# Kernel tuning notes

Hardware: AMD Instinct MI355X
Metric: run time of the kernel (lower is better)

## Reference

```python
import jax, jax.numpy as jnp
import numpy as np

N = 50000      # nodes
E = 250000     # edges
D = 256        # in_channels
MSG = 256      # msg_dim
TD = 64        # time encoder out_channels
ED = MSG + TD  # edge_dim = 320
H = 4          # heads
C = 64         # out_channels // heads


def setup_inputs() -> dict:
    key = jax.random.key(0)
    ks = jax.random.split(key, 16)
    s_d = 1.0 / np.sqrt(D)
    s_e = 1.0 / np.sqrt(ED)
    return {
        "x": jax.random.normal(ks[0], (N, D), jnp.float32),
        "last_update": jax.random.uniform(ks[1], (N,), jnp.float32) * 1000.0,
        "t": jax.random.uniform(ks[2], (E,), jnp.float32) * 1000.0,
        "msg": jax.random.normal(ks[3], (E, MSG), jnp.float32),
        "edge_index": jax.random.randint(ks[4], (2, E), 0, N, jnp.int32),
        # TimeEncoder: Linear(1, TD) followed by cos
        "time_w": jax.random.normal(ks[5], (TD,), jnp.float32),
        "time_b": jax.random.normal(ks[6], (TD,), jnp.float32) * 0.1,
        # TransformerConv linears (weights stored [out, in] like torch)
        "Wq": jax.random.normal(ks[7], (H * C, D), jnp.float32) * s_d,
        "bq": jnp.zeros((H * C,), jnp.float32),
        "Wk": jax.random.normal(ks[8], (H * C, D), jnp.float32) * s_d,
        "bk": jnp.zeros((H * C,), jnp.float32),
        "Wv": jax.random.normal(ks[9], (H * C, D), jnp.float32) * s_d,
        "bv": jnp.zeros((H * C,), jnp.float32),
        "We": jax.random.normal(ks[10], (H * C, ED), jnp.float32) * s_e,  # lin_edge, no bias
        "Wskip": jax.random.normal(ks[11], (H * C, D), jnp.float32) * s_d,
        "bskip": jnp.zeros((H * C,), jnp.float32),
    }


def reference(x, last_update, t, msg, edge_index, time_w, time_b,
              Wq, bq, Wk, bk, Wv, bv, We, Wskip, bskip):
    src = edge_index[0]  # j: message source
    dst = edge_index[1]  # i: message target

    # time encoding: cos(Linear(1, TD)(rel_t))
    rel_t = last_update[src] - t                              # [E]
    rel_t_enc = jnp.cos(rel_t[:, None] * time_w[None, :] + time_b)  # [E, TD]
    edge_attr = jnp.concatenate([rel_t_enc, msg], axis=-1)    # [E, ED]

    # TransformerConv (heads=4, concat=True, root_weight=True, beta=False, eval mode)
    q = (x @ Wq.T + bq).reshape(N, H, C)
    k = (x @ Wk.T + bk).reshape(N, H, C)
    v = (x @ Wv.T + bv).reshape(N, H, C)
    e = (edge_attr @ We.T).reshape(E, H, C)

    k_j = k[src] + e                                           # [E, H, C]
    alpha = jnp.einsum('ehc,ehc->eh', q[dst], k_j) / np.sqrt(C)  # [E, H]

    # segment softmax over incoming edges of each target node
    m = jax.ops.segment_max(alpha, dst, num_segments=N)        # [N, H]
    m = jnp.where(jnp.isfinite(m), m, 0.0)
    ex = jnp.exp(alpha - m[dst])                               # [E, H]
    denom = jax.ops.segment_sum(ex, dst, num_segments=N)       # [N, H]
    alpha = ex / (denom[dst] + 1e-16)                          # [E, H]

    out_e = (v[src] + e) * alpha[:, :, None]                   # [E, H, C]
    out = jax.ops.segment_sum(out_e, dst, num_segments=N)      # [N, H, C]
    out = out.reshape(N, H * C) + (x @ Wskip.T + bskip)        # skip connection
    return out
```

## Files before the change

### kernel.cpp

```cpp
#include <hip/hip_runtime.h>
#include <math.h>

#define NN 50000
#define EE 250000
#define NPAD 50048

typedef float f32x4 __attribute__((ext_vector_type(4)));
typedef __bf16 bf16x8 __attribute__((ext_vector_type(8)));

static __device__ __forceinline__ ushort f2b(float f) {
    unsigned u = __float_as_uint(f);
    unsigned r = (u + 0x7FFFu + ((u >> 16) & 1u)) >> 16;
    return (ushort)r;
}
static __device__ __forceinline__ float b2f(ushort u) {
    return __uint_as_float(((unsigned)u) << 16);
}

__global__ void k_prep_w(const float* __restrict__ Wq, const float* __restrict__ bq,
                         const float* __restrict__ Wk, const float* __restrict__ bk,
                         const float* __restrict__ Wv, const float* __restrict__ bv,
                         const float* __restrict__ Wskip, const float* __restrict__ bskip,
                         const float* __restrict__ We,
                         ushort* __restrict__ Wnb, ushort* __restrict__ Web,
                         float* __restrict__ bcat) {
    int i = blockIdx.x * 256 + threadIdx.x;
    int st = gridDim.x * 256;
    for (int idx = i; idx < 1024 * 256; idx += st) {
        int n = idx >> 8, kk = idx & 255;
        int sel = n >> 8, o = n & 255;
        const float* W = (sel == 0) ? Wq : (sel == 1) ? Wk : (sel == 2) ? Wv : Wskip;
        Wnb[idx] = f2b(W[o * 256 + kk]);
    }
    for (int idx = i; idx < 256 * 320; idx += st) Web[idx] = f2b(We[idx]);
    for (int idx = i; idx < 1024; idx += st) {
        int sel = idx >> 8, o = idx & 255;
        const float* b = (sel == 0) ? bq : (sel == 1) ? bk : (sel == 2) ? bv : bskip;
        bcat[idx] = b[o];
    }
}

__global__ void k_zero(unsigned* __restrict__ deg) {
    int i = blockIdx.x * 256 + threadIdx.x;
    if (i < NN) deg[i] = 0u;
}

__global__ void k_hist(const int* __restrict__ ei, unsigned* __restrict__ deg) {
    int i = blockIdx.x * 256 + threadIdx.x;
    if (i < EE) atomicAdd(&deg[ei[EE + i]], 1u);
}

__global__ __launch_bounds__(1024) void k_scan(const unsigned* __restrict__ deg,
                                               unsigned* __restrict__ offs,
                                               unsigned* __restrict__ cursor) {
    __shared__ unsigned part[1024];
    int t = threadIdx.x;
    const int CH = (NN + 1023) / 1024;
    int b0 = t * CH;
    unsigned s = 0;
    for (int i = 0; i < CH; ++i) { int idx = b0 + i; if (idx < NN) s += deg[idx]; }
    part[t] = s;
    __syncthreads();
    for (int d = 1; d < 1024; d <<= 1) {
        unsigned v = (t >= d) ? part[t - d] : 0u;
        __syncthreads();
        part[t] += v;
        __syncthreads();
    }
    unsigned run = (t == 0) ? 0u : part[t - 1];
    for (int i = 0; i < CH; ++i) {
        int idx = b0 + i;
        if (idx < NN) { offs[idx] = run; cursor[idx] = run; run += deg[idx]; }
    }
    if (t == 1023) offs[NN] = EE;
}

__global__ void k_scatter(const int* __restrict__ ei, unsigned* __restrict__ cursor,
                          int* __restrict__ sorted_e) {
    int i = blockIdx.x * 256 + threadIdx.x;
    if (i < EE) {
        unsigned p = atomicAdd(&cursor[ei[EE + i]], 1u);
        sorted_e[p] = i;
    }
}

__global__ __launch_bounds__(256) void k_node_mfma(
        const float* __restrict__ x, const ushort* __restrict__ Wnb,
        const float* __restrict__ bcat,
        ushort* __restrict__ qb, ushort* __restrict__ kb, ushort* __restrict__ vb,
        float* __restrict__ out) {
    __shared__ ushort As[128 * 64];
    __shared__ ushort Bs[128 * 64];
    int tid = threadIdx.x;
    int lane = tid & 63, wid = tid >> 6;
    int wr = wid >> 1, wc = wid & 1;
    int li = lane & 15, g = lane >> 4;
    int bm = blockIdx.x, bn = blockIdx.y;
    f32x4 acc[4][4] = {};
    for (int k0 = 0; k0 < 256; k0 += 64) {
        __syncthreads();
        #pragma unroll
        for (int i = 0; i < 4; ++i) {
            int ch = tid + i * 256;
            int r = ch >> 3, c = ch & 7;
            int row = bm * 128 + r;
            union { ushort u[8]; uint4 v; } s;
            if (row < NN) {
                const float* xr = x + (size_t)row * 256 + k0 + c * 8;
                float4 a = *(const float4*)xr;
                float4 b = *(const float4*)(xr + 4);
                s.u[0] = f2b(a.x); s.u[1] = f2b(a.y); s.u[2] = f2b(a.z); s.u[3] = f2b(a.w);
                s.u[4] = f2b(b.x); s.u[5] = f2b(b.y); s.u[6] = f2b(b.z); s.u[7] = f2b(b.w);
            } else {
                s.v = make_uint4(0, 0, 0, 0);
            }
            *(uint4*)&As[r * 64 + ((c ^ (r & 7)) * 8)] = s.v;
            uint4 vb4 = *(const uint4*)(Wnb + (size_t)(bn * 128 + r) * 256 + k0 + c * 8);
            *(uint4*)&Bs[r * 64 + ((c ^ (r & 7)) * 8)] = vb4;
        }
        __syncthreads();
        #pragma unroll
        for (int kk = 0; kk < 2; ++kk) {
            bf16x8 a[4], b[4];
            #pragma unroll
            for (int m = 0; m < 4; ++m) {
                int r = wr * 64 + m * 16 + li;
                a[m] = *(const bf16x8*)&As[r * 64 + (((kk * 4 + g) ^ (r & 7)) * 8)];
            }
            #pragma unroll
            for (int n = 0; n < 4; ++n) {
                int r = wc * 64 + n * 16 + li;
                b[n] = *(const bf16x8*)&Bs[r * 64 + (((kk * 4 + g) ^ (r & 7)) * 8)];
            }
            #pragma unroll
            for (int m = 0; m < 4; ++m)
                #pragma unroll
                for (int n = 0; n < 4; ++n)
                    acc[m][n] = __builtin_amdgcn_mfma_f32_16x16x32_bf16(a[m], b[n], acc[m][n], 0, 0, 0);
        }
    }
    int sel = bn >> 1;
    int cbase = (bn & 1) * 128;
    ushort* dstb = (sel == 0) ? qb : (sel == 1) ? kb : vb;
    #pragma unroll
    for (int m = 0; m < 4; ++m) {
        #pragma unroll
        for (int r = 0; r < 4; ++r) {
            int row = bm * 128 + wr * 64 + m * 16 + g * 4 + r;
            if (row >= NN) continue;
            #pragma unroll
            for (int n = 0; n < 4; ++n) {
                int coll = wc * 64 + n * 16 + li;
                float val = acc[m][n][r] + bcat[bn * 128 + coll];
                int cin = cbase + coll;
                if (sel < 3) dstb[(size_t)row * 256 + cin] = f2b(val);
                else         out[(size_t)row * 256 + cin] = val;
            }
        }
    }
}

__global__ __launch_bounds__(256) void k_edge_mfma(
        const float* __restrict__ msg, const float* __restrict__ t_arr,
        const float* __restrict__ lu, const float* __restrict__ tw,
        const float* __restrict__ tb, const ushort* __restrict__ Web,
        const ushort* __restrict__ qb, const ushort* __restrict__ kb,
        const int* __restrict__ ei,
        ushort* __restrict__ ebuf, float* __restrict__ alpha) {
    __shared__ ushort SS[64 * 328];
    __shared__ int s_src[64], s_dst[64];
    __shared__ float s_relt[64];
    int tid = threadIdx.x;
    int lane = tid & 63, wid = tid >> 6;
    int wr = wid >> 1, wc = wid & 1;
    int li = lane & 15, g = lane >> 4;
    int e0 = blockIdx.x * 64;
    if (tid < 64) {
        int e = e0 + tid;
        if (e >= EE) e = EE - 1;
        int s = ei[e];
        s_src[tid] = s;
        s_dst[tid] = ei[EE + e];
        s_relt[tid] = lu[s] - t_arr[e];
    }
    f32x4 acc[2][8] = {};
    for (int k0 = 0; k0 < 320; k0 += 64) {
        __syncthreads();
        #pragma unroll
        for (int i = 0; i < 2; ++i) {
            int ch = tid + i * 256;
            int r = ch >> 3, c = ch & 7;
            union { ushort u[8]; uint4 v; } s;
            if (k0 == 0) {
                float rt = s_relt[r];
                #pragma unroll
                for (int j = 0; j < 8; ++j)
                    s.u[j] = f2b(cosf(rt * tw[c * 8 + j] + tb[c * 8 + j]));
            } else {
                int erow = e0 + r; if (erow >= EE) erow = EE - 1;
                const float* mrow = msg + (size_t)erow * 256 + (k0 - 64) + c * 8;
                float4 a = *(const float4*)mrow;
                float4 b = *(const float4*)(mrow + 4);
                s.u[0] = f2b(a.x); s.u[1] = f2b(a.y); s.u[2] = f2b(a.z); s.u[3] = f2b(a.w);
                s.u[4] = f2b(b.x); s.u[5] = f2b(b.y); s.u[6] = f2b(b.z); s.u[7] = f2b(b.w);
            }
            *(uint4*)&SS[r * 64 + ((c ^ (r & 7)) * 8)] = s.v;
        }
        #pragma unroll
        for (int i = 0; i < 8; ++i) {
            int ch = tid + i * 256;
            int r = ch >> 3, c = ch & 7;
            uint4 vb4 = *(const uint4*)(Web + (size_t)r * 320 + k0 + c * 8);
            *(uint4*)&SS[4096 + r * 64 + ((c ^ (r & 7)) * 8)] = vb4;
        }
        __syncthreads();
        #pragma unroll
        for (int kk = 0; kk < 2; ++kk) {
            bf16x8 a[2], b[8];
            #pragma unroll
            for (int m = 0; m < 2; ++m) {
                int r = wr * 32 + m * 16 + li;
                a[m] = *(const bf16x8*)&SS[r * 64 + (((kk * 4 + g) ^ (r & 7)) * 8)];
            }
            #pragma unroll
            for (int n = 0; n < 8; ++n) {
                int r = wc * 128 + n * 16 + li;
                b[n] = *(const bf16x8*)&SS[4096 + r * 64 + (((kk * 4 + g) ^ (r & 7)) * 8)];
            }
            #pragma unroll
            for (int m = 0; m < 2; ++m)
                #pragma unroll
                for (int n = 0; n < 8; ++n)
                    acc[m][n] = __builtin_amdgcn_mfma_f32_16x16x32_bf16(a[m], b[n], acc[m][n], 0, 0, 0);
        }
    }
    #pragma unroll
    for (int m = 0; m < 2; ++m) {
        #pragma unroll
        for (int r = 0; r < 4; ++r) {
            int el = wr * 32 + m * 16 + g * 4 + r;
            int edge = e0 + el;
            if (edge >= EE) continue;
            #pragma unroll
            for (int n = 0; n < 8; ++n) {
                int col = wc * 128 + n * 16 + li;
                ebuf[(size_t)edge * 256 + col] = f2b(acc[m][n][r]);
            }
        }
    }
    __syncthreads();
    #pragma unroll
    for (int i = 0; i < 8; ++i) {
        int idx = tid + i * 256;
        int r = idx >> 5, c = idx & 31;
        uint4 kv = *(const uint4*)(kb + (size_t)s_src[r] * 256 + c * 8);
        *(uint4*)&SS[r * 328 + c * 8] = kv;
    }
    __syncthreads();
    #pragma unroll
    for (int m = 0; m < 2; ++m)
        #pragma unroll
        for (int r = 0; r < 4; ++r) {
            int el = wr * 32 + m * 16 + g * 4 + r;
            #pragma unroll
            for (int n = 0; n < 8; ++n)
                acc[m][n][r] += b2f(SS[el * 328 + wc * 128 + n * 16 + li]);
        }
    __syncthreads();
    #pragma unroll
    for (int i = 0; i < 8; ++i) {
        int idx = tid + i * 256;
        int r = idx >> 5, c = idx & 31;
        uint4 qv = *(const uint4*)(qb + (size_t)s_dst[r] * 256 + c * 8);
        *(uint4*)&SS[r * 328 + c * 8] = qv;
    }
    __syncthreads();
    #pragma unroll
    for (int m = 0; m < 2; ++m) {
        #pragma unroll
        for (int r = 0; r < 4; ++r) {
            int el = wr * 32 + m * 16 + g * 4 + r;
            int edge = e0 + el;
            float p0 = 0.f, p1 = 0.f;
            #pragma unroll
            for (int n = 0; n < 8; ++n) {
                float qv = b2f(SS[el * 328 + wc * 128 + n * 16 + li]);
                float tt = qv * acc[m][n][r];
                if (n < 4) p0 += tt; else p1 += tt;
            }
            #pragma unroll
            for (int msk = 1; msk < 16; msk <<= 1) {
                p0 += __shfl_xor(p0, msk);
                p1 += __shfl_xor(p1, msk);
            }
            if (li < 2 && edge < EE) {
                float av = ((li == 0) ? p0 : p1) * 0.125f;
                int h = wc * 2 + li;
                alpha[(size_t)edge * 4 + h] = av;
            }
        }
    }
}

__global__ __launch_bounds__(256) void k_gather(
        const ushort* __restrict__ ebuf, const ushort* __restrict__ vb,
        const float* __restrict__ alpha, const int* __restrict__ ei,
        const int* __restrict__ sorted_e, const unsigned* __restrict__ offs,
        float* __restrict__ out) {
    int wid = threadIdx.x >> 6, lane = threadIdx.x & 63;
    int n = blockIdx.x * 4 + wid;
    if (n >= NN) return;
    unsigned p0 = offs[n], p1 = offs[n + 1];
    if (p0 == p1) return;
    int h = lane >> 4;
    int c0 = lane * 4;
    float m = -INFINITY;
    for (unsigned p = p0; p < p1; ++p) {
        int e = sorted_e[p];
        m = fmaxf(m, alpha[(size_t)e * 4 + h]);
    }
    f32x4 acc = {0.f, 0.f, 0.f, 0.f};
    float denom = 0.f;
    for (unsigned p = p0; p < p1; ++p) {
        int e = sorted_e[p];
        int src = ei[e];
        float ex = __expf(alpha[(size_t)e * 4 + h] - m);
        ushort4 ev = *(const ushort4*)(ebuf + (size_t)e * 256 + c0);
        ushort4 vv = *(const ushort4*)(vb + (size_t)src * 256 + c0);
        acc[0] += (b2f(vv.x) + b2f(ev.x)) * ex;
        acc[1] += (b2f(vv.y) + b2f(ev.y)) * ex;
        acc[2] += (b2f(vv.z) + b2f(ev.z)) * ex;
        acc[3] += (b2f(vv.w) + b2f(ev.w)) * ex;
        denom += ex;
    }
    float inv = 1.f / (denom + 1e-16f);
    float4 o = *(float4*)(out + (size_t)n * 256 + c0);
    o.x += acc[0] * inv;
    o.y += acc[1] * inv;
    o.z += acc[2] * inv;
    o.w += acc[3] * inv;
    *(float4*)(out + (size_t)n * 256 + c0) = o;
}

extern "C" void kernel_launch(void* const* d_in, const int* in_sizes, int n_in,
                              void* d_out, int out_size, void* d_ws, size_t ws_size,
                              hipStream_t stream) {
    const float* x        = (const float*)d_in[0];
    const float* last_upd = (const float*)d_in[1];
    const float* t_arr    = (const float*)d_in[2];
    const float* msg      = (const float*)d_in[3];
    const int*   ei       = (const int*)d_in[4];
    const float* time_w   = (const float*)d_in[5];
    const float* time_b   = (const float*)d_in[6];
    const float* Wq = (const float*)d_in[7];  const float* bq = (const float*)d_in[8];
    const float* Wk = (const float*)d_in[9];  const float* bk = (const float*)d_in[10];
    const float* Wv = (const float*)d_in[11]; const float* bv = (const float*)d_in[12];
    const float* We = (const float*)d_in[13];
    const float* Wsk = (const float*)d_in[14]; const float* bsk = (const float*)d_in[15];
    float* out = (float*)d_out;
    char* base = (char*)d_ws;

    size_t off = 0;
    auto carve = [&](size_t bytes) {
        void* p = base + off;
        off += (bytes + 255) & ~(size_t)255;
        return p;
    };
    ushort* Wnb   = (ushort*)carve((size_t)1024 * 256 * 2);
    ushort* Web   = (ushort*)carve((size_t)256 * 320 * 2);
    float*  bcat  = (float*) carve(1024 * 4);
    ushort* qb    = (ushort*)carve((size_t)NN * 256 * 2);
    ushort* kb    = (ushort*)carve((size_t)NN * 256 * 2);
    ushort* vb    = (ushort*)carve((size_t)NN * 256 * 2);
    ushort* ebuf  = (ushort*)carve((size_t)EE * 256 * 2);
    float*  alpha = (float*) carve((size_t)EE * 4 * 4);
    unsigned* deg    = (unsigned*)carve((size_t)NN * 4);
    unsigned* cursor = (unsigned*)carve((size_t)NN * 4);
    unsigned* offs   = (unsigned*)carve((size_t)(NN + 1) * 4);
    int*      sorted = (int*)     carve((size_t)EE * 4);

    k_prep_w<<<dim3(512), dim3(256), 0, stream>>>(Wq, bq, Wk, bk, Wv, bv, Wsk, bsk, We,
                                                  Wnb, Web, bcat);
    k_zero<<<dim3((NN + 255) / 256), dim3(256), 0, stream>>>(deg);
    k_hist<<<dim3((EE + 255) / 256), dim3(256), 0, stream>>>(ei, deg);
    k_scan<<<dim3(1), dim3(1024), 0, stream>>>(deg, offs, cursor);
    k_scatter<<<dim3((EE + 255) / 256), dim3(256), 0, stream>>>(ei, cursor, sorted);
    k_node_mfma<<<dim3(391, 8), dim3(256), 0, stream>>>(x, Wnb, bcat, qb, kb, vb, out);
    k_edge_mfma<<<dim3(3907), dim3(256), 0, stream>>>(msg, t_arr, last_upd,
                                                      time_w, time_b, Web, qb, kb, ei,
                                                      ebuf, alpha);
    k_gather<<<dim3((NN + 3) / 4), dim3(256), 0, stream>>>(ebuf, vb, alpha, ei,
                                                           sorted, offs, out);
}
```

Measured before the change: 621.0 us.

## Fold v[src] into edge buffer and compute q·k separately in edge kernel

Result: slower. 671.5 us (+8.1%).

```diff
diff --git a/kernel.cpp b/kernel.cpp
--- a/kernel.cpp
+++ b/kernel.cpp
@@ -3,7 +3,6 @@
 
 #define NN 50000
 #define EE 250000
-#define NPAD 50048
 
 typedef float f32x4 __attribute__((ext_vector_type(4)));
 typedef __bf16 bf16x8 __attribute__((ext_vector_type(8)));
@@ -160,22 +159,23 @@
     }
 }
 
-__global__ __launch_bounds__(256) void k_edge_mfma(
+__global__ __launch_bounds__(512, 2) void k_edge_mfma(
         const float* __restrict__ msg, const float* __restrict__ t_arr,
         const float* __restrict__ lu, const float* __restrict__ tw,
         const float* __restrict__ tb, const ushort* __restrict__ Web,
         const ushort* __restrict__ qb, const ushort* __restrict__ kb,
-        const int* __restrict__ ei,
+        const ushort* __restrict__ vb, const int* __restrict__ ei,
         ushort* __restrict__ ebuf, float* __restrict__ alpha) {
-    __shared__ ushort SS[64 * 328];
-    __shared__ int s_src[64], s_dst[64];
-    __shared__ float s_relt[64];
+    __shared__ ushort SS[24576];
+    __shared__ int s_src[128], s_dst[128];
+    __shared__ float s_relt[128];
+    __shared__ float s_qk[128][4];
     int tid = threadIdx.x;
     int lane = tid & 63, wid = tid >> 6;
     int wr = wid >> 1, wc = wid & 1;
     int li = lane & 15, g = lane >> 4;
-    int e0 = blockIdx.x * 64;
-    if (tid < 64) {
+    int e0 = blockIdx.x * 128;
+    if (tid < 128) {
         int e = e0 + tid;
         if (e >= EE) e = EE - 1;
         int s = ei[e];
@@ -183,12 +183,28 @@
         s_dst[tid] = ei[EE + e];
         s_relt[tid] = lu[s] - t_arr[e];
     }
+    __syncthreads();
+    {
+        int el = tid >> 2, h = tid & 3;
+        const ushort* qr = qb + (size_t)s_dst[el] * 256 + h * 64;
+        const ushort* kr = kb + (size_t)s_src[el] * 256 + h * 64;
+        float s = 0.f;
+        #pragma unroll
+        for (int c = 0; c < 8; ++c) {
+            union { ushort u[8]; uint4 v; } uq, uk;
+            uq.v = *(const uint4*)(qr + c * 8);
+            uk.v = *(const uint4*)(kr + c * 8);
+            #pragma unroll
+            for (int j = 0; j < 8; ++j) s += b2f(uq.u[j]) * b2f(uk.u[j]);
+        }
+        s_qk[el][h] = s;
+    }
     f32x4 acc[2][8] = {};
     for (int k0 = 0; k0 < 320; k0 += 64) {
         __syncthreads();
         #pragma unroll
         for (int i = 0; i < 2; ++i) {
-            int ch = tid + i * 256;
+            int ch = tid + i * 512;
             int r = ch >> 3, c = ch & 7;
             union { ushort u[8]; uint4 v; } s;
             if (k0 == 0) {
@@ -207,11 +223,11 @@
             *(uint4*)&SS[r * 64 + ((c ^ (r & 7)) * 8)] = s.v;
         }
         #pragma unroll
-        for (int i = 0; i < 8; ++i) {
-            int ch = tid + i * 256;
+        for (int i = 0; i < 4; ++i) {
+            int ch = tid + i * 512;
             int r = ch >> 3, c = ch & 7;
             uint4 vb4 = *(const uint4*)(Web + (size_t)r * 320 + k0 + c * 8);
-            *(uint4*)&SS[4096 + r * 64 + ((c ^ (r & 7)) * 8)] = vb4;
+            *(uint4*)&SS[8192 + r * 64 + ((c ^ (r & 7)) * 8)] = vb4;
         }
         __syncthreads();
         #pragma unroll
@@ -225,7 +241,7 @@
             #pragma unroll
             for (int n = 0; n < 8; ++n) {
                 int r = wc * 128 + n * 16 + li;
-                b[n] = *(const bf16x8*)&SS[4096 + r * 64 + (((kk * 4 + g) ^ (r & 7)) * 8)];
+                b[n] = *(const bf16x8*)&SS[8192 + r * 64 + (((kk * 4 + g) ^ (r & 7)) * 8)];
             }
             #pragma unroll
             for (int m = 0; m < 2; ++m)
@@ -235,76 +251,76 @@
         }
     }
     #pragma unroll
-    for (int m = 0; m < 2; ++m) {
-        #pragma unroll
-        for (int r = 0; r < 4; ++r) {
-            int el = wr * 32 + m * 16 + g * 4 + r;
-            int edge = e0 + el;
-            if (edge >= EE) continue;
-            #pragma unroll
-            for (int n = 0; n < 8; ++n) {
-                int col = wc * 128 + n * 16 + li;
-                ebuf[(size_t)edge * 256 + col] = f2b(acc[m][n][r]);
-            }
-        }
-    }
-    __syncthreads();
-    #pragma unroll
-    for (int i = 0; i < 8; ++i) {
-        int idx = tid + i * 256;
-        int r = idx >> 5, c = idx & 31;
-        uint4 kv = *(const uint4*)(kb + (size_t)s_src[r] * 256 + c * 8);
-        *(uint4*)&SS[r * 328 + c * 8] = kv;
-    }
-    __syncthreads();
-    #pragma unroll
-    for (int m = 0; m < 2; ++m)
-        #pragma unroll
-        for (int r = 0; r < 4; ++r) {
-            int el = wr * 32 + m * 16 + g * 4 + r;
-            #pragma unroll
-            for (int n = 0; n < 8; ++n)
-                acc[m][n][r] += b2f(SS[el * 328 + wc * 128 + n * 16 + li]);
-        }
-    __syncthreads();
-    #pragma unroll
-    for (int i = 0; i < 8; ++i) {
-        int idx = tid + i * 256;
-        int r = idx >> 5, c = idx & 31;
-        uint4 qv = *(const uint4*)(qb + (size_t)s_dst[r] * 256 + c * 8);
-        *(uint4*)&SS[r * 328 + c * 8] = qv;
-    }
-    __syncthreads();
-    #pragma unroll
-    for (int m = 0; m < 2; ++m) {
-        #pragma unroll
-        for (int r = 0; r < 4; ++r) {
-            int el = wr * 32 + m * 16 + g * 4 + r;
-            int edge = e0 + el;
-            float p0 = 0.f, p1 = 0.f;
-            #pragma unroll
-            for (int n = 0; n < 8; ++n) {
-                float qv = b2f(SS[el * 328 + wc * 128 + n * 16 + li]);
-                float tt = qv * acc[m][n][r];
-                if (n < 4) p0 += tt; else p1 += tt;
-            }
-            #pragma unroll
-            for (int msk = 1; msk < 16; msk <<= 1) {
-                p0 += __shfl_xor(p0, msk);
-                p1 += __shfl_xor(p1, msk);
-            }
-            if (li < 2 && edge < EE) {
-                float av = ((li == 0) ? p0 : p1) * 0.125f;
-                int h = wc * 2 + li;
-                alpha[(size_t)edge * 4 + h] = av;
+    for (int h2 = 0; h2 < 2; ++h2) {
+        __syncthreads();
+        #pragma unroll
+        for (int i = 0; i < 4; ++i) {
+            int ch = tid + i * 512;
+            int r = ch >> 5, c = ch & 31;
+            uint4 qv = *(const uint4*)(qb + (size_t)s_dst[h2 * 64 + r] * 256 + c * 8);
+            *(uint4*)&SS[r * 328 + c * 8] = qv;
+        }
+        __syncthreads();
+        if ((wr >> 1) == h2) {
+            int wrl = wr & 1;
+            #pragma unroll
+            for (int m = 0; m < 2; ++m) {
+                #pragma unroll
+                for (int r = 0; r < 4; ++r) {
+                    int el = wrl * 32 + m * 16 + g * 4 + r;
+                    float p0 = 0.f, p1 = 0.f;
+                    #pragma unroll
+                    for (int n = 0; n < 8; ++n) {
+                        float qv = b2f(SS[el * 328 + wc * 128 + n * 16 + li]);
+                        float tt = qv * acc[m][n][r];
+                        if (n < 4) p0 += tt; else p1 += tt;
+                    }
+                    #pragma unroll
+                    for (int msk = 1; msk < 16; msk <<= 1) {
+                        p0 += __shfl_xor(p0, msk);
+                        p1 += __shfl_xor(p1, msk);
+                    }
+                    int edge = e0 + h2 * 64 + el;
+                    if (li < 2 && edge < EE) {
+                        int h = wc * 2 + li;
+                        float av = (((li == 0) ? p0 : p1) + s_qk[h2 * 64 + el][h]) * 0.125f;
+                        alpha[(size_t)edge * 4 + h] = av;
+                    }
+                }
+            }
+        }
+        __syncthreads();
+        #pragma unroll
+        for (int i = 0; i < 4; ++i) {
+            int ch = tid + i * 512;
+            int r = ch >> 5, c = ch & 31;
+            uint4 vv = *(const uint4*)(vb + (size_t)s_src[h2 * 64 + r] * 256 + c * 8);
+            *(uint4*)&SS[r * 328 + c * 8] = vv;
+        }
+        __syncthreads();
+        if ((wr >> 1) == h2) {
+            int wrl = wr & 1;
+            #pragma unroll
+            for (int m = 0; m < 2; ++m) {
+                #pragma unroll
+                for (int r = 0; r < 4; ++r) {
+                    int el = wrl * 32 + m * 16 + g * 4 + r;
+                    int edge = e0 + h2 * 64 + el;
+                    if (edge >= EE) continue;
+                    #pragma unroll
+                    for (int n = 0; n < 8; ++n) {
+                        int col = wc * 128 + n * 16 + li;
+                        ebuf[(size_t)edge * 256 + col] =
+                            f2b(acc[m][n][r] + b2f(SS[el * 328 + col]));
+                    }
+                }
             }
         }
     }
 }
 
 __global__ __launch_bounds__(256) void k_gather(
-        const ushort* __restrict__ ebuf, const ushort* __restrict__ vb,
-        const float* __restrict__ alpha, const int* __restrict__ ei,
+        const ushort* __restrict__ ebuf, const float* __restrict__ alpha,
         const int* __restrict__ sorted_e, const unsigned* __restrict__ offs,
         float* __restrict__ out) {
     int wid = threadIdx.x >> 6, lane = threadIdx.x & 63;
@@ -323,14 +339,12 @@
     float denom = 0.f;
     for (unsigned p = p0; p < p1; ++p) {
         int e = sorted_e[p];
-        int src = ei[e];
         float ex = __expf(alpha[(size_t)e * 4 + h] - m);
         ushort4 ev = *(const ushort4*)(ebuf + (size_t)e * 256 + c0);
-        ushort4 vv = *(const ushort4*)(vb + (size_t)src * 256 + c0);
-        acc[0] += (b2f(vv.x) + b2f(ev.x)) * ex;
-        acc[1] += (b2f(vv.y) + b2f(ev.y)) * ex;
-        acc[2] += (b2f(vv.z) + b2f(ev.z)) * ex;
-        acc[3] += (b2f(vv.w) + b2f(ev.w)) * ex;
+        acc[0] += b2f(ev.x) * ex;
+        acc[1] += b2f(ev.y) * ex;
+        acc[2] += b2f(ev.z) * ex;
+        acc[3] += b2f(ev.w) * ex;
         denom += ex;
     }
     float inv = 1.f / (denom + 1e-16f);
@@ -386,9 +400,8 @@
     k_scan<<<dim3(1), dim3(1024), 0, stream>>>(deg, offs, cursor);
     k_scatter<<<dim3((EE + 255) / 256), dim3(256), 0, stream>>>(ei, cursor, sorted);
     k_node_mfma<<<dim3(391, 8), dim3(256), 0, stream>>>(x, Wnb, bcat, qb, kb, vb, out);
-    k_edge_mfma<<<dim3(3907), dim3(256), 0, stream>>>(msg, t_arr, last_upd,
-                                                      time_w, time_b, Web, qb, kb, ei,
-                                                      ebuf, alpha);
-    k_gather<<<dim3((NN + 3) / 4), dim3(256), 0, stream>>>(ebuf, vb, alpha, ei,
+    k_edge_mfma<<<dim3((EE + 127) / 128), dim3(512), 0, stream>>>(
+        msg, t_arr, last_upd, time_w, time_b, Web, qb, kb, vb, ei, ebuf, alpha);
+    k_gather<<<dim3((NN + 3) / 4), dim3(256), 0, stream>>>(ebuf, alpha,
                                                            sorted, offs, out);
 }
```

## Fold v[src] into edge buffer and write edge data in destination-sorted order

Applied to the files above, without the earlier changes.

New measurement: 584.4 us. 5.9% less time.

```diff
diff --git a/kernel.cpp b/kernel.cpp
--- a/kernel.cpp
+++ b/kernel.cpp
@@ -3,15 +3,13 @@
 
 #define NN 50000
 #define EE 250000
-#define NPAD 50048
 
 typedef float f32x4 __attribute__((ext_vector_type(4)));
 typedef __bf16 bf16x8 __attribute__((ext_vector_type(8)));
 
 static __device__ __forceinline__ ushort f2b(float f) {
-    unsigned u = __float_as_uint(f);
-    unsigned r = (u + 0x7FFFu + ((u >> 16) & 1u)) >> 16;
-    return (ushort)r;
+    __bf16 h = (__bf16)f;
+    return *(ushort*)&h;
 }
 static __device__ __forceinline__ float b2f(ushort u) {
     return __uint_as_float(((unsigned)u) << 16);
@@ -76,11 +74,11 @@
 }
 
 __global__ void k_scatter(const int* __restrict__ ei, unsigned* __restrict__ cursor,
-                          int* __restrict__ sorted_e) {
+                          int* __restrict__ rank) {
     int i = blockIdx.x * 256 + threadIdx.x;
     if (i < EE) {
         unsigned p = atomicAdd(&cursor[ei[EE + i]], 1u);
-        sorted_e[p] = i;
+        rank[i] = (int)p;
     }
 }
 
@@ -165,10 +163,11 @@
         const float* __restrict__ lu, const float* __restrict__ tw,
         const float* __restrict__ tb, const ushort* __restrict__ Web,
         const ushort* __restrict__ qb, const ushort* __restrict__ kb,
-        const int* __restrict__ ei,
+        const ushort* __restrict__ vb, const int* __restrict__ ei,
+        const int* __restrict__ rank,
         ushort* __restrict__ ebuf, float* __restrict__ alpha) {
     __shared__ ushort SS[64 * 328];
-    __shared__ int s_src[64], s_dst[64];
+    __shared__ int s_src[64], s_dst[64], s_rank[64];
     __shared__ float s_relt[64];
     int tid = threadIdx.x;
     int lane = tid & 63, wid = tid >> 6;
@@ -181,6 +180,7 @@
         int s = ei[e];
         s_src[tid] = s;
         s_dst[tid] = ei[EE + e];
+        s_rank[tid] = rank[e];
         s_relt[tid] = lu[s] - t_arr[e];
     }
     f32x4 acc[2][8] = {};
@@ -234,6 +234,15 @@
                     acc[m][n] = __builtin_amdgcn_mfma_f32_16x16x32_bf16(a[m], b[n], acc[m][n], 0, 0, 0);
         }
     }
+    __syncthreads();
+    #pragma unroll
+    for (int i = 0; i < 8; ++i) {
+        int idx = tid + i * 256;
+        int r = idx >> 5, c = idx & 31;
+        uint4 vv = *(const uint4*)(vb + (size_t)s_src[r] * 256 + c * 8);
+        *(uint4*)&SS[r * 328 + c * 8] = vv;
+    }
+    __syncthreads();
     #pragma unroll
     for (int m = 0; m < 2; ++m) {
         #pragma unroll
@@ -241,10 +250,11 @@
             int el = wr * 32 + m * 16 + g * 4 + r;
             int edge = e0 + el;
             if (edge >= EE) continue;
+            size_t rb = (size_t)s_rank[el] * 256;
             #pragma unroll
             for (int n = 0; n < 8; ++n) {
                 int col = wc * 128 + n * 16 + li;
-                ebuf[(size_t)edge * 256 + col] = f2b(acc[m][n][r]);
+                ebuf[rb + col] = f2b(acc[m][n][r] + b2f(SS[el * 328 + col]));
             }
         }
     }
@@ -296,17 +306,15 @@
             if (li < 2 && edge < EE) {
                 float av = ((li == 0) ? p0 : p1) * 0.125f;
                 int h = wc * 2 + li;
-                alpha[(size_t)edge * 4 + h] = av;
+                alpha[(size_t)s_rank[el] * 4 + h] = av;
             }
         }
     }
 }
 
 __global__ __launch_bounds__(256) void k_gather(
-        const ushort* __restrict__ ebuf, const ushort* __restrict__ vb,
-        const float* __restrict__ alpha, const int* __restrict__ ei,
-        const int* __restrict__ sorted_e, const unsigned* __restrict__ offs,
-        float* __restrict__ out) {
+        const ushort* __restrict__ ebuf, const float* __restrict__ alpha,
+        const unsigned* __restrict__ offs, float* __restrict__ out) {
     int wid = threadIdx.x >> 6, lane = threadIdx.x & 63;
     int n = blockIdx.x * 4 + wid;
     if (n >= NN) return;
@@ -315,22 +323,17 @@
     int h = lane >> 4;
     int c0 = lane * 4;
     float m = -INFINITY;
-    for (unsigned p = p0; p < p1; ++p) {
-        int e = sorted_e[p];
-        m = fmaxf(m, alpha[(size_t)e * 4 + h]);
-    }
+    for (unsigned p = p0; p < p1; ++p)
+        m = fmaxf(m, alpha[(size_t)p * 4 + h]);
     f32x4 acc = {0.f, 0.f, 0.f, 0.f};
     float denom = 0.f;
     for (unsigned p = p0; p < p1; ++p) {
-        int e = sorted_e[p];
-        int src = ei[e];
-        float ex = __expf(alpha[(size_t)e * 4 + h] - m);
-        ushort4 ev = *(const ushort4*)(ebuf + (size_t)e * 256 + c0);
-        ushort4 vv = *(const ushort4*)(vb + (size_t)src * 256 + c0);
-        acc[0] += (b2f(vv.x) + b2f(ev.x)) * ex;
-        acc[1] += (b2f(vv.y) + b2f(ev.y)) * ex;
-        acc[2] += (b2f(vv.z) + b2f(ev.z)) * ex;
-        acc[3] += (b2f(vv.w) + b2f(ev.w)) * ex;
+        float ex = __expf(alpha[(size_t)p * 4 + h] - m);
+        ushort4 ev = *(const ushort4*)(ebuf + (size_t)p * 256 + c0);
+        acc[0] += b2f(ev.x) * ex;
+        acc[1] += b2f(ev.y) * ex;
+        acc[2] += b2f(ev.z) * ex;
+        acc[3] += b2f(ev.w) * ex;
         denom += ex;
     }
     float inv = 1.f / (denom + 1e-16f);
@@ -377,18 +380,16 @@
     unsigned* deg    = (unsigned*)carve((size_t)NN * 4);
     unsigned* cursor = (unsigned*)carve((size_t)NN * 4);
     unsigned* offs   = (unsigned*)carve((size_t)(NN + 1) * 4);
-    int*      sorted = (int*)     carve((size_t)EE * 4);
+    int*      rank   = (int*)     carve((size_t)EE * 4);
 
     k_prep_w<<<dim3(512), dim3(256), 0, stream>>>(Wq, bq, Wk, bk, Wv, bv, Wsk, bsk, We,
                                                   Wnb, Web, bcat);
     k_zero<<<dim3((NN + 255) / 256), dim3(256), 0, stream>>>(deg);
     k_hist<<<dim3((EE + 255) / 256), dim3(256), 0, stream>>>(ei, deg);
     k_scan<<<dim3(1), dim3(1024), 0, stream>>>(deg, offs, cursor);
-    k_scatter<<<dim3((EE + 255) / 256), dim3(256), 0, stream>>>(ei, cursor, sorted);
+    k_scatter<<<dim3((EE + 255) / 256), dim3(256), 0, stream>>>(ei, cursor, rank);
     k_node_mfma<<<dim3(391, 8), dim3(256), 0, stream>>>(x, Wnb, bcat, qb, kb, vb, out);
-    k_edge_mfma<<<dim3(3907), dim3(256), 0, stream>>>(msg, t_arr, last_upd,
-                                                      time_w, time_b, Web, qb, kb, ei,
-                                                      ebuf, alpha);
-    k_gather<<<dim3((NN + 3) / 4), dim3(256), 0, stream>>>(ebuf, vb, alpha, ei,
-                                                           sorted, offs, out);
-}
+    k_edge_mfma<<<dim3((EE + 63) / 64), dim3(256), 0, stream>>>(
+        msg, t_arr, last_upd, time_w, time_b, Web, qb, kb, vb, ei, rank, ebuf, alpha);
+    k_gather<<<dim3((NN + 3) / 4), dim3(256), 0, stream>>>(ebuf, alpha, offs, out);
+}
```
